# Kernel optimization log

Measured on AMD Instinct MI355X. Metric: run time of the kernel, lower is better.

The kernel has to match this reference:

```python
import jax, jax.numpy as jnp
import numpy as np

DIM, HEADS, HD = 256, 8, 32
WS, GT, SR = 8, 1, 2
B_, H0, W0 = 4, 128, 128
SCALE = HD ** -0.5


def _bilinear_up_align(x, s):
    # x: (B, C, h, w) -> (B, C, h*s, w*s), bilinear, align_corners=True (matches torch)
    B, C, h, w = x.shape
    oh, ow = h * s, w * s
    def coords(n, o):
        pos = jnp.arange(o, dtype=jnp.float32) * ((n - 1) / (o - 1))
        i0 = jnp.clip(jnp.floor(pos).astype(jnp.int32), 0, n - 2)
        t = pos - i0.astype(jnp.float32)
        return i0, t
    y0, ty = coords(h, oh)
    x0, tx = coords(w, ow)
    top = x[:, :, y0, :] * (1 - ty)[:, None] + x[:, :, y0 + 1, :] * ty[:, None]
    return top[:, :, :, x0] * (1 - tx) + top[:, :, :, x0 + 1] * tx


def _layernorm(x, w, b, eps=1e-5):
    mu = x.mean(-1, keepdims=True)
    var = x.var(-1, keepdims=True)
    return (x - mu) * jax.lax.rsqrt(var + eps) * w + b


def setup_inputs() -> dict:
    key = jax.random.key(0)
    ks = jax.random.split(key, 8)
    w = lambda k, shape: jax.random.normal(k, shape, jnp.float32) * 0.02
    return {
        "x": jax.random.normal(ks[0], (B_, H0 * W0, DIM), jnp.float32),
        "gt": jax.random.normal(ks[1], (B_, H0 // WS, W0 // WS, GT, DIM), jnp.float32),
        "q_w": w(ks[2], (DIM, DIM)), "q_b": jnp.zeros((DIM,), jnp.float32),
        "kv_w": w(ks[3], (2 * DIM, DIM)), "kv_b": jnp.zeros((2 * DIM,), jnp.float32),
        "sr_w": w(ks[4], (DIM, DIM, SR, SR)), "sr_b": jnp.zeros((DIM,), jnp.float32),
        "norm_w": jnp.ones((DIM,), jnp.float32), "norm_b": jnp.zeros((DIM,), jnp.float32),
        "proj_w": w(ks[5], (DIM, DIM)), "proj_b": jnp.zeros((DIM,), jnp.float32),
        "H": H0, "W": W0,
    }


def reference(x, gt, q_w, q_b, kv_w, kv_b, sr_w, sr_b, norm_w, norm_b, proj_w, proj_b, H, W):
    Bb, Np, C = x.shape
    nH, nW = H // WS, W // WS  # H, W multiples of WS -> no padding branch
    xm = x.reshape(Bb, H, W, C)
    # window partition -> (B, WS*WS, C), B = Bb*nH*nW
    xw = xm.reshape(Bb, nH, WS, nW, WS, C).transpose(0, 1, 3, 2, 4, 5).reshape(-1, WS * WS, C)
    g = gt.reshape(-1, GT, C)  # gt grid already matches (nH, nW)
    skip = g
    xc = jnp.concatenate([g, xw], axis=1)  # (B, N, C), N = GT + WS*WS
    B, N, _ = xc.shape
    q = (xc @ q_w.T + q_b).reshape(B, N, HEADS, HD).transpose(0, 2, 1, 3)  # (B,h,N,d)
    # spatial-reduction KV branch (sr_ratio > 1, gt_num != 0)
    x_ = xw.transpose(0, 2, 1).reshape(B, C, WS, WS)
    x_ = _bilinear_up_align(x_, SR)  # (B, C, WS*SR, WS*SR)
    x_ = jax.lax.conv_general_dilated(
        x_, sr_w, (SR, SR), "VALID",
        dimension_numbers=("NCHW", "OIHW", "NCHW")) + sr_b[None, :, None, None]  # (B,C,WS,WS)
    x_ = _layernorm(x_.reshape(B, C, -1).transpose(0, 2, 1), norm_w, norm_b)
    x_ = jnp.concatenate([g, x_], axis=1)  # (B, N, C)
    kv = (x_ @ kv_w.T + kv_b).reshape(B, -1, 2, HEADS, HD).transpose(2, 0, 3, 1, 4)
    k, v = kv[0], kv[1]  # (B,h,N,d)
    attn = jax.nn.softmax(jnp.einsum("bhnd,bhmd->bhnm", q, k) * SCALE, axis=-1)
    out = jnp.einsum("bhnm,bhmd->bhnd", attn, v).transpose(0, 2, 1, 3).reshape(B, N, C)
    out = out @ proj_w.T + proj_b
    gt_out = out[:, :GT, :]
    xo = out[:, GT:, :].reshape(Bb, nH, nW, WS, WS, C)
    xo = xo.transpose(0, 1, 3, 2, 4, 5).reshape(Bb, H, W, C)  # window reverse
    return xo.reshape(Bb, H * W, C), gt_out, skip
```

## Files before the change

### kernel.cpp

```cpp
#include <hip/hip_runtime.h>

typedef __attribute__((ext_vector_type(4))) float f32x4;
typedef __attribute__((ext_vector_type(8))) float f32x8;
typedef __attribute__((ext_vector_type(8))) short bf16x8;
typedef __attribute__((ext_vector_type(2))) uint u32x2;

#define SCALE_ 0.17677669529663687f

__device__ __forceinline__ float bf2f(ushort u){
  union { unsigned i; float f; } v; v.i = ((unsigned)u) << 16; return v.f;
}
__device__ __forceinline__ ushort f2bf(float f){
  union { float f; unsigned i; } v; v.f = f;
  unsigned r = v.i + 0x7fffu + ((v.i >> 16) & 1u);
  return (ushort)(r >> 16);
}
__device__ __forceinline__ void gl16(const void* g, const ushort* l) {
  __builtin_amdgcn_global_load_lds((const __attribute__((address_space(1))) uint*)g,
                                   (__attribute__((address_space(3))) uint*)l, 16, 0, 0);
}

__global__ __launch_bounds__(256) void k_prep(const float* __restrict__ x,
    const float* __restrict__ gt, ushort* __restrict__ xc,
    ushort* __restrict__ xkv, float* __restrict__ out2)
{
  int row = blockIdx.x;
  int c = threadIdx.x;
  int wi = row / 65, n = row - wi * 65;
  if (n == 0) {
    float g = gt[(size_t)wi * 256 + c];
    ushort gb = f2bf(g);
    xc[(size_t)row * 256 + c] = gb;
    xkv[(size_t)row * 256 + c] = gb;
    out2[(size_t)wi * 256 + c] = g;
  } else {
    int s = n - 1, r = s >> 3, cc = s & 7;
    int b = wi >> 8, wh = (wi >> 4) & 15, ww = wi & 15;
    int hw = (wh * 8 + r) * 128 + ww * 8 + cc;
    xc[(size_t)row * 256 + c] = f2bf(x[((size_t)b * 16384 + hw) * 256 + c]);
  }
}

__global__ __launch_bounds__(256) void k_wprep(const float* __restrict__ qw,
    const float* __restrict__ kvw, const float* __restrict__ pw,
    const float* __restrict__ srw, ushort* __restrict__ wq,
    ushort* __restrict__ wkv, ushort* __restrict__ wpr, ushort* __restrict__ wcv)
{
  int i = blockIdx.x * 256 + threadIdx.x;
  if (i < 65536)            wq[i] = f2bf(qw[i]);
  else if (i < 196608)      wkv[i - 65536] = f2bf(kvw[i - 65536]);
  else if (i < 262144)      wpr[i - 196608] = f2bf(pw[i - 196608]);
  else {
    int j = i - 262144;
    int o = j >> 10, t = (j >> 8) & 3, cc = j & 255;
    wcv[j] = f2bf(srw[o * 1024 + cc * 4 + t]);
  }
}

template<int N>
__global__ __launch_bounds__(256) void k_gemm2(const ushort* __restrict__ A,
    const ushort* __restrict__ W, const float* __restrict__ bias,
    ushort* __restrict__ C)
{
  constexpr int K = 256;
  __shared__ __align__(16) ushort As[2][128 * 64];
  __shared__ __align__(16) ushort Bs[2][128 * 64];
  int lin = blockIdx.y * gridDim.x + blockIdx.x;
  int qq = (gridDim.x * gridDim.y) >> 3;
  int sw2 = (lin & 7) * qq + (lin >> 3);
  int m0 = (sw2 / gridDim.x) * 128, n0 = (sw2 % gridDim.x) * 128;
  int tid = threadIdx.x, lane = tid & 63;
  int wave = tid >> 6;
  int lm = lane & 15, kg = lane >> 4;
  int wr = wave >> 1, wc = wave & 1;

  const char* Ab = (const char*)A + (size_t)m0 * (K * 2);
  const char* Bb = (const char*)W + (size_t)n0 * (K * 2);

  auto stage = [&](int buf, int kt) {
#pragma unroll
    for (int j = 0; j < 4; ++j) {
      int c = j * 256 + tid;
      int row = c >> 3, slot = c & 7;
      int srcoff = row * (K * 2) + kt * 128 + ((slot * 16) ^ ((row & 7) << 4));
      gl16(Ab + srcoff, (const ushort*)((const char*)As[buf] + c * 16));
      gl16(Bb + srcoff, (const ushort*)((const char*)Bs[buf] + c * 16));
    }
  };

  f32x4 acc[4][4];
  f32x4 zero = {0.f, 0.f, 0.f, 0.f};
#pragma unroll
  for (int a = 0; a < 4; ++a)
#pragma unroll
    for (int b = 0; b < 4; ++b) acc[a][b] = zero;

  stage(0, 0);
  __syncthreads();
#pragma unroll
  for (int t = 0; t < 4; ++t) {
    int cur = t & 1;
    if (t < 3) stage(cur ^ 1, t + 1);
#pragma unroll
    for (int s = 0; s < 2; ++s) {
      int sw = (lm & 7) << 4;
      bf16x8 af[4], bw[4];
#pragma unroll
      for (int mi = 0; mi < 4; ++mi) {
        int row = wr * 64 + mi * 16 + lm;
        af[mi] = *(const bf16x8*)((const char*)As[cur] + row * 128 + ((s * 64 + kg * 16) ^ sw));
      }
#pragma unroll
      for (int ni = 0; ni < 4; ++ni) {
        int row = wc * 64 + ni * 16 + lm;
        bw[ni] = *(const bf16x8*)((const char*)Bs[cur] + row * 128 + ((s * 64 + kg * 16) ^ sw));
      }
#pragma unroll
      for (int mi = 0; mi < 4; ++mi)
#pragma unroll
        for (int ni = 0; ni < 4; ++ni)
          acc[mi][ni] = __builtin_amdgcn_mfma_f32_16x16x32_bf16(af[mi], bw[ni], acc[mi][ni], 0, 0, 0);
    }
    __syncthreads();
  }

  int rbase = m0 + wr * 64 + kg * 4;
#pragma unroll
  for (int ni = 0; ni < 4; ++ni) {
    int col = n0 + wc * 64 + ni * 16 + lm;
    float bv = bias[col];
#pragma unroll
    for (int mi = 0; mi < 4; ++mi) {
#pragma unroll
      for (int r = 0; r < 4; ++r)
        C[(size_t)(rbase + mi * 16 + r) * N + col] = f2bf(acc[mi][ni][r] + bv);
    }
  }
}

__device__ __forceinline__ f32x8 row_lerp(const char* srcS, int row, int cg, float ty) {
  int a0 = row * 512 + ((cg * 16) ^ ((row & 7) << 4));
  int a1 = (row + 8) * 512 + ((cg * 16) ^ ((row & 7) << 4));
  bf16x8 a = *(const bf16x8*)(srcS + a0);
  bf16x8 b = *(const bf16x8*)(srcS + a1);
  f32x8 h;
#pragma unroll
  for (int e = 0; e < 8; ++e) {
    float av = bf2f((ushort)a[e]);
    h[e] = av + ty * (bf2f((ushort)b[e]) - av);
  }
  return h;
}
__device__ __forceinline__ void emit_u(char* U, const f32x8& Ha, const f32x8& Hb,
                                       float tx, int s, int cg) {
  bf16x8 o8;
#pragma unroll
  for (int e = 0; e < 8; ++e) {
    float lv = Ha[e];
    o8[e] = (short)f2bf(lv + tx * (Hb[e] - lv));
  }
  *(bf16x8*)(U + s * 512 + ((cg * 16) ^ ((s & 7) << 4))) = o8;
}

template<int XH, int DX>
__device__ __forceinline__ void conv_build(const char* srcS, char* U,
                                           int dy, int i, int cg)
{
  int yy = 2 * i + dy;
  float py = yy * (7.0f / 15.0f);
  int iy = (int)py; if (iy > 6) iy = 6;
  float ty = py - iy;
  constexpr int j0 = XH * 3;
  int rb = iy * 8 + j0;
  f32x8 H0 = row_lerp(srcS, rb + 0, cg, ty);
  f32x8 H1 = row_lerp(srcS, rb + 1, cg, ty);
  f32x8 H2 = row_lerp(srcS, rb + 2, cg, ty);
  f32x8 H3 = row_lerp(srcS, rb + 3, cg, ty);
  f32x8 H4 = row_lerp(srcS, rb + 4, cg, ty);
  int sb = i * 8 + XH * 4;
  if (XH == 0 && DX == 0) {
    emit_u(U, H0, H1, 0.0f,        sb + 0, cg);
    emit_u(U, H0, H1, 14.f / 15.f, sb + 1, cg);
    emit_u(U, H1, H2, 13.f / 15.f, sb + 2, cg);
    emit_u(U, H2, H3, 12.f / 15.f, sb + 3, cg);
  } else if (XH == 0 && DX == 1) {
    emit_u(U, H0, H1,  7.f / 15.f, sb + 0, cg);
    emit_u(U, H1, H2,  6.f / 15.f, sb + 1, cg);
    emit_u(U, H2, H3,  5.f / 15.f, sb + 2, cg);
    emit_u(U, H3, H4,  4.f / 15.f, sb + 3, cg);
  } else if (XH == 1 && DX == 0) {
    emit_u(U, H0, H1, 11.f / 15.f, sb + 0, cg);
    emit_u(U, H1, H2, 10.f / 15.f, sb + 1, cg);
    emit_u(U, H2, H3,  9.f / 15.f, sb + 2, cg);
    emit_u(U, H3, H4,  8.f / 15.f, sb + 3, cg);
  } else {
    emit_u(U, H1, H2,  3.f / 15.f, sb + 0, cg);
    emit_u(U, H2, H3,  2.f / 15.f, sb + 1, cg);
    emit_u(U, H3, H4,  1.f / 15.f, sb + 2, cg);
    emit_u(U, H3, H4,  1.0f,       sb + 3, cg);
  }
}

__global__ __launch_bounds__(512)
__attribute__((amdgpu_waves_per_eu(4, 4)))
void k_conv(const ushort* __restrict__ xc,
    const ushort* __restrict__ wconv, ushort* __restrict__ cconv)
{
  __shared__ __align__(16) ushort srcS[64 * 256];
  __shared__ __align__(16) ushort Ubuf[64 * 256];
  int wi = blockIdx.x;
  int tid = threadIdx.x, wave = tid >> 6, lane = tid & 63;
  int lm = lane & 15, kg = lane >> 4;

  const char* src_g = (const char*)(xc + (size_t)(wi * 65 + 1) * 256);
#pragma unroll
  for (int j = 0; j < 4; ++j) {
    int c = j * 512 + tid;
    int row = c >> 5, slot = c & 31;
    int srcoff = row * 512 + ((slot * 16) ^ ((row & 7) << 4));
    gl16(src_g + srcoff, (const ushort*)((const char*)srcS + c * 16));
  }

  f32x4 acc[4][2];
  f32x4 zero = {0.f, 0.f, 0.f, 0.f};
#pragma unroll
  for (int a = 0; a < 4; a++)
#pragma unroll
    for (int b = 0; b < 2; b++) acc[a][b] = zero;

  int cg = tid & 31;
  int i = (tid >> 5) & 7;
  int xh = tid >> 8;

  auto mfma_tap = [&](int t) {
    const ushort* wc = wconv + t * 256;
    for (int kk = 0; kk < 256; kk += 32) {
      int kb = kk + kg * 8;
      bf16x8 afr[4];
#pragma unroll
      for (int mi = 0; mi < 4; mi++) {
        int srow = mi * 16 + lm;
        int off = (srow * 512 + 2 * kb) ^ ((srow & 7) << 4);
        afr[mi] = *(const bf16x8*)((const char*)Ubuf + off);
      }
#pragma unroll
      for (int ni = 0; ni < 2; ni++) {
        bf16x8 b = *(const bf16x8*)(wc + (size_t)(wave * 32 + ni * 16 + lm) * 1024 + kb);
#pragma unroll
        for (int mi = 0; mi < 4; mi++)
          acc[mi][ni] = __builtin_amdgcn_mfma_f32_16x16x32_bf16(afr[mi], b, acc[mi][ni], 0, 0, 0);
      }
    }
  };

  __syncthreads();

  if (xh == 0) conv_build<0, 0>((const char*)srcS, (char*)Ubuf, 0, i, cg);
  else         conv_build<1, 0>((const char*)srcS, (char*)Ubuf, 0, i, cg);
  __syncthreads();
  mfma_tap(0);
  __syncthreads();
  if (xh == 0) conv_build<0, 1>((const char*)srcS, (char*)Ubuf, 0, i, cg);
  else         conv_build<1, 1>((const char*)srcS, (char*)Ubuf, 0, i, cg);
  __syncthreads();
  mfma_tap(1);
  __syncthreads();
  if (xh == 0) conv_build<0, 0>((const char*)srcS, (char*)Ubuf, 1, i, cg);
  else         conv_build<1, 0>((const char*)srcS, (char*)Ubuf, 1, i, cg);
  __syncthreads();
  mfma_tap(2);
  __syncthreads();
  if (xh == 0) conv_build<0, 1>((const char*)srcS, (char*)Ubuf, 1, i, cg);
  else         conv_build<1, 1>((const char*)srcS, (char*)Ubuf, 1, i, cg);
  __syncthreads();
  mfma_tap(3);

#pragma unroll
  for (int mi = 0; mi < 4; mi++) {
    int row = wi * 64 + mi * 16 + kg * 4;
#pragma unroll
    for (int ni = 0; ni < 2; ni++) {
      int col = wave * 32 + ni * 16 + lm;
#pragma unroll
      for (int r = 0; r < 4; r++)
        cconv[(size_t)(row + r) * 256 + col] = f2bf(acc[mi][ni][r]);
    }
  }
}

__global__ __launch_bounds__(256) void k_ln(const ushort* __restrict__ cconv,
    const float* __restrict__ srb, const float* __restrict__ nw,
    const float* __restrict__ nb, ushort* __restrict__ xkv)
{
  int row = blockIdx.x * 4 + (threadIdx.x >> 6);
  int lane = threadIdx.x & 63;
  const ushort* p = cconv + (size_t)row * 256;
  float v[4]; float sum = 0.f, sq = 0.f;
#pragma unroll
  for (int r = 0; r < 4; r++) {
    int c = r * 64 + lane;
    v[r] = bf2f(p[c]) + srb[c];
    sum += v[r]; sq += v[r] * v[r];
  }
#pragma unroll
  for (int off = 1; off < 64; off <<= 1) {
    sum += __shfl_xor(sum, off, 64);
    sq  += __shfl_xor(sq,  off, 64);
  }
  float mean = sum * (1.f / 256.f);
  float var = sq * (1.f / 256.f) - mean * mean;
  float rs = rsqrtf(var + 1e-5f);
  int wi = row >> 6, s = row & 63;
  ushort* o = xkv + (size_t)(wi * 65 + 1 + s) * 256;
#pragma unroll
  for (int r = 0; r < 4; r++) {
    int c = r * 64 + lane;
    o[c] = f2bf((v[r] - mean) * rs * nw[c] + nb[c]);
  }
}

__global__ __launch_bounds__(256) void k_attn(const ushort* __restrict__ q,
    const ushort* __restrict__ kv, ushort* __restrict__ att)
{
  __shared__ ushort smem[4][8064];
  int wi = blockIdx.x >> 1;
  int tid = threadIdx.x, wave = tid >> 6, lane = tid & 63;
  int h = (blockIdx.x & 1) * 4 + wave;
  int lm = lane & 15, kg = lane >> 4;
  ushort* plds = smem[wave];
  ushort* vt   = smem[wave] + 5760;

  size_t qbase  = (size_t)wi * 65 * 256 + (size_t)h * 32;
  size_t kvbase = (size_t)wi * 65 * 512 + (size_t)h * 32;

  for (int e = lane; e < 2080; e += 64) {
    int m = e >> 5, d = e & 31;
    vt[d * 72 + m] = kv[kvbase + (size_t)m * 512 + 256 + d];
  }

  bf16x8 akf[5], bqf[5];
#pragma unroll
  for (int i = 0; i < 5; i++) {
    akf[i] = *(const bf16x8*)(kv + kvbase + (size_t)(16 * i + lm) * 512 + kg * 8);
    bqf[i] = *(const bf16x8*)(q  + qbase  + (size_t)(16 * i + lm) * 256 + kg * 8);
  }

  f32x4 sc[5][5];
  f32x4 zero = {0.f, 0.f, 0.f, 0.f};
#pragma unroll
  for (int mi = 0; mi < 5; mi++)
#pragma unroll
    for (int nj = 0; nj < 5; nj++) sc[mi][nj] = zero;
#pragma unroll
  for (int mi = 0; mi < 5; mi++)
#pragma unroll
    for (int nj = 0; nj < 5; nj++)
      sc[mi][nj] = __builtin_amdgcn_mfma_f32_16x16x32_bf16(akf[mi], bqf[nj], sc[mi][nj], 0, 0, 0);

  const float C = SCALE_ * 1.4426950408889634f;
  float inv[5], p64b[5];
#pragma unroll
  for (int nj = 0; nj < 5; nj++) {
    float s4 = sc[4][nj][0];
    float mx = (kg == 0) ? s4 : -1e30f;
#pragma unroll
    for (int mi = 0; mi < 4; mi++)
#pragma unroll
      for (int r = 0; r < 4; r++) mx = fmaxf(mx, sc[mi][nj][r]);
    mx = fmaxf(mx, __shfl_xor(mx, 16, 64));
    mx = fmaxf(mx, __shfl_xor(mx, 32, 64));
    float sum = 0.f;
#pragma unroll
    for (int mi = 0; mi < 4; mi++)
#pragma unroll
      for (int r = 0; r < 4; r++) {
        float e = exp2f((sc[mi][nj][r] - mx) * C);
        sc[mi][nj][r] = e; sum += e;
      }
    float e4 = exp2f((s4 - mx) * C);
    sum += (kg == 0) ? e4 : 0.f;
    sum += __shfl_xor(sum, 16, 64);
    sum += __shfl_xor(sum, 32, 64);
    inv[nj] = 1.0f / sum;
    p64b[nj] = __shfl(e4, lm, 64);
  }

#pragma unroll
  for (int nj = 0; nj < 5; nj++) {
    int n = 16 * nj + lm;
#pragma unroll
    for (int mi = 0; mi < 4; mi++) {
      uint lo = (uint)f2bf(sc[mi][nj][0]) | ((uint)f2bf(sc[mi][nj][1]) << 16);
      uint hi = (uint)f2bf(sc[mi][nj][2]) | ((uint)f2bf(sc[mi][nj][3]) << 16);
      u32x2 pk = {lo, hi};
      *(u32x2*)(plds + n * 72 + 16 * mi + 4 * kg) = pk;
    }
  }

  f32x4 od[2][5];
#pragma unroll
  for (int dt = 0; dt < 2; dt++)
#pragma unroll
    for (int nj = 0; nj < 5; nj++) od[dt][nj] = zero;
#pragma unroll
  for (int c = 0; c < 2; c++) {
    bf16x8 av[2], bp[5];
#pragma unroll
    for (int dt = 0; dt < 2; dt++)
      av[dt] = *(const bf16x8*)(vt + (16 * dt + lm) * 72 + c * 32 + kg * 8);
#pragma unroll
    for (int nj = 0; nj < 5; nj++)
      bp[nj] = *(const bf16x8*)(plds + (16 * nj + lm) * 72 + c * 32 + kg * 8);
#pragma unroll
    for (int dt = 0; dt < 2; dt++)
#pragma unroll
      for (int nj = 0; nj < 5; nj++)
        od[dt][nj] = __builtin_amdgcn_mfma_f32_16x16x32_bf16(av[dt], bp[nj], od[dt][nj], 0, 0, 0);
  }
  float v64[8];
#pragma unroll
  for (int dt = 0; dt < 2; dt++)
#pragma unroll
    for (int r = 0; r < 4; r++)
      v64[dt * 4 + r] = bf2f(vt[(16 * dt + 4 * kg + r) * 72 + 64]);
#pragma unroll
  for (int dt = 0; dt < 2; dt++)
#pragma unroll
    for (int nj = 0; nj < 5; nj++)
#pragma unroll
      for (int r = 0; r < 4; r++)
        od[dt][nj][r] += v64[dt * 4 + r] * p64b[nj];

#pragma unroll
  for (int nj = 0; nj < 5; nj++) {
    int n = 16 * nj + lm;
    float scl = inv[nj];
#pragma unroll
    for (int dt = 0; dt < 2; dt++) {
      uint lo = (uint)f2bf(od[dt][nj][0] * scl) | ((uint)f2bf(od[dt][nj][1] * scl) << 16);
      uint hi = (uint)f2bf(od[dt][nj][2] * scl) | ((uint)f2bf(od[dt][nj][3] * scl) << 16);
      u32x2 pk = {lo, hi};
      *(u32x2*)(plds + n * 40 + 16 * dt + 4 * kg) = pk;
    }
  }
  size_t abase = (size_t)wi * 65 * 256 + (size_t)h * 32;
  for (int e = lane; e < 1040; e += 64) {
    int n = e >> 4, d2 = e & 15;
    *(uint*)(att + abase + (size_t)n * 256 + 2 * d2) = *(const uint*)(plds + n * 40 + 2 * d2);
  }
}

__global__ __launch_bounds__(256) void k_scatter(const ushort* __restrict__ po,
    float* __restrict__ out)
{
  size_t e = (size_t)blockIdx.x * 256 + threadIdx.x;
  if (e < 16777216) {
    int c = (int)(e & 255);
    int hw = (int)((e >> 8) & 16383);
    int b = (int)(e >> 22);
    int hh = hw >> 7, wp = hw & 127;
    int wh = hh >> 3, r = hh & 7, ww = wp >> 3, cc = wp & 7;
    int wi = b * 256 + wh * 16 + ww;
    int n = 1 + r * 8 + cc;
    out[e] = bf2f(po[(size_t)(wi * 65 + n) * 256 + c]);
  } else {
    size_t e2 = e - 16777216;
    int wi = (int)(e2 >> 8), c = (int)(e2 & 255);
    out[e] = bf2f(po[(size_t)(wi * 65) * 256 + c]);
  }
}

extern "C" void kernel_launch(void* const* d_in, const int* in_sizes, int n_in,
                              void* d_out, int out_size, void* d_ws, size_t ws_size,
                              hipStream_t stream)
{
  const float* x    = (const float*)d_in[0];
  const float* gt   = (const float*)d_in[1];
  const float* q_w  = (const float*)d_in[2];
  const float* q_b  = (const float*)d_in[3];
  const float* kv_w = (const float*)d_in[4];
  const float* kv_b = (const float*)d_in[5];
  const float* sr_w = (const float*)d_in[6];
  const float* sr_b = (const float*)d_in[7];
  const float* nw   = (const float*)d_in[8];
  const float* nb   = (const float*)d_in[9];
  const float* p_w  = (const float*)d_in[10];
  const float* p_b  = (const float*)d_in[11];
  (void)in_sizes; (void)n_in; (void)out_size;

  if (ws_size < 204996608u) return;
  char* ws = (char*)d_ws;
  ushort* xc  = (ushort*)(ws);
  ushort* qb  = (ushort*)(ws + 34078720);
  ushort* xkv = (ushort*)(ws + 68157440);
  ushort* kv  = (ushort*)(ws + 102236160);
  ushort* ccv = (ushort*)(ws + 170393600);
  ushort* wq  = (ushort*)(ws + 203948032);
  ushort* wkv = (ushort*)(ws + 204079104);
  ushort* wpr = (ushort*)(ws + 204341248);
  ushort* wcv = (ushort*)(ws + 204472320);

  float* out = (float*)d_out;
  float* out2 = out + 16777216 + 262144;

  k_prep<<<66560, 256, 0, stream>>>(x, gt, xc, xkv, out2);
  k_wprep<<<2048, 256, 0, stream>>>(q_w, kv_w, p_w, sr_w, wq, wkv, wpr, wcv);
  k_gemm2<256><<<dim3(2, 520), 256, 0, stream>>>(xc, wq, q_b, qb);
  k_conv<<<1024, 512, 0, stream>>>(xc, wcv, ccv);
  k_ln<<<16384, 256, 0, stream>>>(ccv, sr_b, nw, nb, xkv);
  k_gemm2<512><<<dim3(4, 520), 256, 0, stream>>>(xkv, wkv, kv_b, kv);
  k_attn<<<2048, 256, 0, stream>>>(qb, kv, xc);
  k_gemm2<256><<<dim3(2, 520), 256, 0, stream>>>(xc, wpr, p_b, qb);
  k_scatter<<<66560, 256, 0, stream>>>(qb, out);
}
```

Measured before the change: 274.0 us.

## Fuse LayerNorm into conv epilogue and window-reverse scatter into projection GEMM

The LayerNorm is folded into the conv kernel's epilogue, with row statistics reduced through shuffles and LDS, so the bf16 conv intermediate no longer goes through a global round trip. The output projection GEMM now writes fp32 results straight to their window-reversed positions in the output, which removes the separate scatter kernel and its extra read and write of the projected activations. The cost is added epilogue work and synchronisation in the conv kernel, plus strided fp32 stores with integer division in the GEMM epilogue. The fused path also keeps the projection output in fp32 instead of rounding it to bf16 first.

```diff
diff --git a/kernel.cpp b/kernel.cpp
--- a/kernel.cpp
+++ b/kernel.cpp
@@ -134,6 +134,99 @@
 #pragma unroll
       for (int r = 0; r < 4; ++r)
         C[(size_t)(rbase + mi * 16 + r) * N + col] = f2bf(acc[mi][ni][r] + bv);
+    }
+  }
+}
+
+__global__ __launch_bounds__(256) void k_gemm_out(const ushort* __restrict__ A,
+    const ushort* __restrict__ W, const float* __restrict__ bias,
+    float* __restrict__ out)
+{
+  constexpr int K = 256, N = 256;
+  __shared__ __align__(16) ushort As[2][128 * 64];
+  __shared__ __align__(16) ushort Bs[2][128 * 64];
+  int lin = blockIdx.y * gridDim.x + blockIdx.x;
+  int qq = (gridDim.x * gridDim.y) >> 3;
+  int sw2 = (lin & 7) * qq + (lin >> 3);
+  int m0 = (sw2 / gridDim.x) * 128, n0 = (sw2 % gridDim.x) * 128;
+  int tid = threadIdx.x, lane = tid & 63;
+  int wave = tid >> 6;
+  int lm = lane & 15, kg = lane >> 4;
+  int wr = wave >> 1, wc = wave & 1;
+
+  const char* Ab = (const char*)A + (size_t)m0 * (K * 2);
+  const char* Bb = (const char*)W + (size_t)n0 * (K * 2);
+
+  auto stage = [&](int buf, int kt) {
+#pragma unroll
+    for (int j = 0; j < 4; ++j) {
+      int c = j * 256 + tid;
+      int row = c >> 3, slot = c & 7;
+      int srcoff = row * (K * 2) + kt * 128 + ((slot * 16) ^ ((row & 7) << 4));
+      gl16(Ab + srcoff, (const ushort*)((const char*)As[buf] + c * 16));
+      gl16(Bb + srcoff, (const ushort*)((const char*)Bs[buf] + c * 16));
+    }
+  };
+
+  f32x4 acc[4][4];
+  f32x4 zero = {0.f, 0.f, 0.f, 0.f};
+#pragma unroll
+  for (int a = 0; a < 4; ++a)
+#pragma unroll
+    for (int b = 0; b < 4; ++b) acc[a][b] = zero;
+
+  stage(0, 0);
+  __syncthreads();
+#pragma unroll
+  for (int t = 0; t < 4; ++t) {
+    int cur = t & 1;
+    if (t < 3) stage(cur ^ 1, t + 1);
+#pragma unroll
+    for (int s = 0; s < 2; ++s) {
+      int sw = (lm & 7) << 4;
+      bf16x8 af[4], bw[4];
+#pragma unroll
+      for (int mi = 0; mi < 4; ++mi) {
+        int row = wr * 64 + mi * 16 + lm;
+        af[mi] = *(const bf16x8*)((const char*)As[cur] + row * 128 + ((s * 64 + kg * 16) ^ sw));
+      }
+#pragma unroll
+      for (int ni = 0; ni < 4; ++ni) {
+        int row = wc * 64 + ni * 16 + lm;
+        bw[ni] = *(const bf16x8*)((const char*)Bs[cur] + row * 128 + ((s * 64 + kg * 16) ^ sw));
+      }
+#pragma unroll
+      for (int mi = 0; mi < 4; ++mi)
+#pragma unroll
+        for (int ni = 0; ni < 4; ++ni)
+          acc[mi][ni] = __builtin_amdgcn_mfma_f32_16x16x32_bf16(af[mi], bw[ni], acc[mi][ni], 0, 0, 0);
+    }
+    __syncthreads();
+  }
+
+  int rbase = m0 + wr * 64 + kg * 4;
+#pragma unroll
+  for (int mi = 0; mi < 4; ++mi) {
+#pragma unroll
+    for (int r = 0; r < 4; ++r) {
+      int g = rbase + mi * 16 + r;
+      int wi2 = g / 65;
+      int n = g - wi2 * 65;
+      size_t dstrow;
+      if (n == 0) {
+        dstrow = (size_t)(16777216 >> 8) + wi2;
+      } else {
+        int s = n - 1;
+        int b = wi2 >> 8, wh = (wi2 >> 4) & 15, ww = wi2 & 15;
+        int r2 = s >> 3, cc = s & 7;
+        dstrow = (size_t)(b << 14) + (wh * 8 + r2) * 128 + ww * 8 + cc;
+      }
+      float* dst = out + dstrow * 256;
+#pragma unroll
+      for (int ni = 0; ni < 4; ++ni) {
+        int col = n0 + wc * 64 + ni * 16 + lm;
+        dst[col] = acc[mi][ni][r] + bias[col];
+      }
     }
   }
 }
@@ -201,10 +294,10 @@
   }
 }
 
-__global__ __launch_bounds__(512)
-__attribute__((amdgpu_waves_per_eu(4, 4)))
-void k_conv(const ushort* __restrict__ xc,
-    const ushort* __restrict__ wconv, ushort* __restrict__ cconv)
+__global__ __launch_bounds__(512, 4)
+void k_conv(const ushort* __restrict__ xc, const ushort* __restrict__ wconv,
+    const float* __restrict__ srb, const float* __restrict__ nw,
+    const float* __restrict__ nb, ushort* __restrict__ xkv)
 {
   __shared__ __align__(16) ushort srcS[64 * 256];
   __shared__ __align__(16) ushort Ubuf[64 * 256];
@@ -275,47 +368,59 @@
   __syncthreads();
   mfma_tap(3);
 
-#pragma unroll
-  for (int mi = 0; mi < 4; mi++) {
-    int row = wi * 64 + mi * 16 + kg * 4;
-#pragma unroll
-    for (int ni = 0; ni < 2; ni++) {
-      int col = wave * 32 + ni * 16 + lm;
-#pragma unroll
-      for (int r = 0; r < 4; r++)
-        cconv[(size_t)(row + r) * 256 + col] = f2bf(acc[mi][ni][r]);
-    }
-  }
-}
-
-__global__ __launch_bounds__(256) void k_ln(const ushort* __restrict__ cconv,
-    const float* __restrict__ srb, const float* __restrict__ nw,
-    const float* __restrict__ nb, ushort* __restrict__ xkv)
-{
-  int row = blockIdx.x * 4 + (threadIdx.x >> 6);
-  int lane = threadIdx.x & 63;
-  const ushort* p = cconv + (size_t)row * 256;
-  float v[4]; float sum = 0.f, sq = 0.f;
-#pragma unroll
-  for (int r = 0; r < 4; r++) {
-    int c = r * 64 + lane;
-    v[r] = bf2f(p[c]) + srb[c];
-    sum += v[r]; sq += v[r] * v[r];
-  }
-#pragma unroll
-  for (int off = 1; off < 64; off <<= 1) {
-    sum += __shfl_xor(sum, off, 64);
-    sq  += __shfl_xor(sq,  off, 64);
-  }
-  float mean = sum * (1.f / 256.f);
-  float var = sq * (1.f / 256.f) - mean * mean;
-  float rs = rsqrtf(var + 1e-5f);
-  int wi = row >> 6, s = row & 63;
-  ushort* o = xkv + (size_t)(wi * 65 + 1 + s) * 256;
-#pragma unroll
-  for (int r = 0; r < 4; r++) {
-    int c = r * 64 + lane;
-    o[c] = f2bf((v[r] - mean) * rs * nw[c] + nb[c]);
+  __syncthreads();
+  float2* stats = (float2*)Ubuf;
+  float2* m2 = (float2*)((char*)Ubuf + 4096);
+
+  float sb0 = srb[wave * 32 + lm];
+  float sb1 = srb[wave * 32 + 16 + lm];
+
+#pragma unroll
+  for (int mi = 0; mi < 4; ++mi) {
+#pragma unroll
+    for (int r = 0; r < 4; ++r) {
+      float v0 = acc[mi][0][r] + sb0;
+      float v1 = acc[mi][1][r] + sb1;
+      float s = v0 + v1, q = v0 * v0 + v1 * v1;
+#pragma unroll
+      for (int off = 1; off < 16; off <<= 1) {
+        s += __shfl_xor(s, off, 64);
+        q += __shfl_xor(q, off, 64);
+      }
+      if (lm == mi * 4 + r) {
+        int row = mi * 16 + kg * 4 + r;
+        stats[row * 8 + wave] = make_float2(s, q);
+      }
+    }
+  }
+  __syncthreads();
+  if (tid < 64) {
+    float s = 0.f, q = 0.f;
+#pragma unroll
+    for (int w = 0; w < 8; ++w) {
+      float2 p = stats[tid * 8 + w];
+      s += p.x; q += p.y;
+    }
+    float mean = s * (1.f / 256.f);
+    float var = q * (1.f / 256.f) - mean * mean;
+    m2[tid] = make_float2(mean, rsqrtf(var + 1e-5f));
+  }
+  __syncthreads();
+
+  float nw0 = nw[wave * 32 + lm],      nb0 = nb[wave * 32 + lm];
+  float nw1 = nw[wave * 32 + 16 + lm], nb1 = nb[wave * 32 + 16 + lm];
+  ushort* orow = xkv + (size_t)(wi * 65 + 1) * 256;
+#pragma unroll
+  for (int mi = 0; mi < 4; ++mi) {
+#pragma unroll
+    for (int r = 0; r < 4; ++r) {
+      int row = mi * 16 + kg * 4 + r;
+      float2 mv = m2[row];
+      float v0 = (acc[mi][0][r] + sb0 - mv.x) * mv.y * nw0 + nb0;
+      float v1 = (acc[mi][1][r] + sb1 - mv.x) * mv.y * nw1 + nb1;
+      orow[(size_t)row * 256 + wave * 32 + lm]      = f2bf(v0);
+      orow[(size_t)row * 256 + wave * 32 + 16 + lm] = f2bf(v1);
+    }
   }
 }
 
@@ -447,26 +552,6 @@
   for (int e = lane; e < 1040; e += 64) {
     int n = e >> 4, d2 = e & 15;
     *(uint*)(att + abase + (size_t)n * 256 + 2 * d2) = *(const uint*)(plds + n * 40 + 2 * d2);
-  }
-}
-
-__global__ __launch_bounds__(256) void k_scatter(const ushort* __restrict__ po,
-    float* __restrict__ out)
-{
-  size_t e = (size_t)blockIdx.x * 256 + threadIdx.x;
-  if (e < 16777216) {
-    int c = (int)(e & 255);
-    int hw = (int)((e >> 8) & 16383);
-    int b = (int)(e >> 22);
-    int hh = hw >> 7, wp = hw & 127;
-    int wh = hh >> 3, r = hh & 7, ww = wp >> 3, cc = wp & 7;
-    int wi = b * 256 + wh * 16 + ww;
-    int n = 1 + r * 8 + cc;
-    out[e] = bf2f(po[(size_t)(wi * 65 + n) * 256 + c]);
-  } else {
-    size_t e2 = e - 16777216;
-    int wi = (int)(e2 >> 8), c = (int)(e2 & 255);
-    out[e] = bf2f(po[(size_t)(wi * 65) * 256 + c]);
   }
 }
 
@@ -494,7 +579,6 @@
   ushort* qb  = (ushort*)(ws + 34078720);
   ushort* xkv = (ushort*)(ws + 68157440);
   ushort* kv  = (ushort*)(ws + 102236160);
-  ushort* ccv = (ushort*)(ws + 170393600);
   ushort* wq  = (ushort*)(ws + 203948032);
   ushort* wkv = (ushort*)(ws + 204079104);
   ushort* wpr = (ushort*)(ws + 204341248);
@@ -506,10 +590,8 @@
   k_prep<<<66560, 256, 0, stream>>>(x, gt, xc, xkv, out2);
   k_wprep<<<2048, 256, 0, stream>>>(q_w, kv_w, p_w, sr_w, wq, wkv, wpr, wcv);
   k_gemm2<256><<<dim3(2, 520), 256, 0, stream>>>(xc, wq, q_b, qb);
-  k_conv<<<1024, 512, 0, stream>>>(xc, wcv, ccv);
-  k_ln<<<16384, 256, 0, stream>>>(ccv, sr_b, nw, nb, xkv);
+  k_conv<<<1024, 512, 0, stream>>>(xc, wcv, sr_b, nw, nb, xkv);
   k_gemm2<512><<<dim3(4, 520), 256, 0, stream>>>(xkv, wkv, kv_b, kv);
   k_attn<<<2048, 256, 0, stream>>>(qb, kv, xc);
-  k_gemm2<256><<<dim3(2, 520), 256, 0, stream>>>(xc, wpr, p_b, qb);
-  k_scatter<<<66560, 256, 0, stream>>>(qb, out);
-}
+  k_gemm_out<<<dim3(2, 520), 256, 0, stream>>>(xc, wpr, p_b, out);
+}
```

New measurement: 265.0 us. 3.3% less time.
